# Performance work log

Measured on AMD Instinct MI355X. Metric: run time of the kernel, lower is better.

## Reference

```python
import jax, jax.numpy as jnp
import numpy as np

E, D, H, T = 8, 1024, 2816, 16384


def setup_inputs() -> dict:
    key = jax.random.key(0)
    k1, k2, k3, k4 = jax.random.split(key, 4)
    x = jax.random.normal(k1, (T, D), dtype=jnp.float32)
    # Params sized per init (w1/w3: [E, H, D], w2: [E, D, H]), trunc-normal-ish scale 0.02
    w1 = 0.02 * jax.random.normal(k2, (E, H, D), dtype=jnp.float32)
    w2 = 0.02 * jax.random.normal(k3, (E, D, H), dtype=jnp.float32)
    w3 = 0.02 * jax.random.normal(k4, (E, H, D), dtype=jnp.float32)
    # Per-expert token counts summing to < T (tail rows are padding, output zeros)
    rng = np.random.default_rng(0)
    props = rng.dirichlet(4.0 * np.ones(E))
    counts = np.floor(props * (T - 64)).astype(np.int32)
    num_tokens_per_expert = jnp.asarray(counts, dtype=jnp.int32)
    return {"x": x, "w1": w1, "w2": w2, "w3": w3,
            "num_tokens_per_expert": num_tokens_per_expert}


def reference(x, w1, w2, w3, num_tokens_per_expert):
    # Tokens are grouped contiguously by expert; grouped GEMM via lax.ragged_dot.
    g = num_tokens_per_expert.astype(jnp.int32)
    # rhs for ragged_dot must be [groups, k, n]
    h1 = jax.lax.ragged_dot(x, jnp.swapaxes(w1, 1, 2), g)   # [T, H] = x @ w1[e].T
    h3 = jax.lax.ragged_dot(x, jnp.swapaxes(w3, 1, 2), g)   # [T, H]
    h = jax.nn.silu(h1) * h3                                # SwiGLU
    out = jax.lax.ragged_dot(h, jnp.swapaxes(w2, 1, 2), g)  # [T, D]
    # Rows beyond sum(counts) are padding -> zeros, matching torch vstack of zeros
    valid = jnp.arange(x.shape[0]) < jnp.sum(g)
    return jnp.where(valid[:, None], out, jnp.zeros((), dtype=out.dtype))
```

## Files before the change

kernel.cpp:

```cpp
#include <hip/hip_runtime.h>

#define NE 8
#define DD 1024
#define HH 2816
#define TT 16384
#define MT (TT / 128 + NE)

constexpr int NJA = MT * (HH / 64);
constexpr int NJB = MT * (DD / 128);
constexpr int ZBLK = 64;

typedef __bf16 bf16;
typedef __bf16 bf16x4 __attribute__((ext_vector_type(4)));
typedef __bf16 bf16x8 __attribute__((ext_vector_type(8)));
typedef float f32x4 __attribute__((ext_vector_type(4)));

constexpr size_t HBUF_E = (size_t)TT * HH;
constexpr size_t XN = (size_t)TT * DD;
constexpr size_t WN = (size_t)NE * HH * DD;
constexpr size_t XB_OFF = HBUF_E * 2;
constexpr size_t W1B_OFF = XB_OFF + XN * 2;
constexpr size_t W3B_OFF = W1B_OFF + WN * 2;

__device__ __forceinline__ void gld16(const void* g, void* l) {
  __builtin_amdgcn_global_load_lds(
      (const __attribute__((address_space(1))) void*)g,
      (__attribute__((address_space(3))) void*)l, 16, 0, 0);
}

__device__ __forceinline__ f32x4 mfma16(bf16x8 a, bf16x8 b, f32x4 c) {
  return __builtin_amdgcn_mfma_f32_16x16x32_bf16(a, b, c, 0, 0, 0);
}

#define BARRIER()                      \
  do {                                 \
    __builtin_amdgcn_s_barrier();      \
    asm volatile("" ::: "memory");     \
  } while (0)

__global__ __launch_bounds__(256) void cvt3_k(
    const float4* __restrict__ x, const float4* __restrict__ w1,
    const float4* __restrict__ w3, bf16x4* __restrict__ xb,
    bf16x4* __restrict__ w1b, bf16x4* __restrict__ w3b) {
  constexpr int NBX = (int)(XN / 4 / 256);
  constexpr int NBW = (int)(WN / 4 / 256);
  int b = blockIdx.x;
  const float4* src;
  bf16x4* dst;
  int i;
  if (b < NBX) {
    src = x; dst = xb; i = b * 256 + threadIdx.x;
  } else if (b < NBX + NBW) {
    src = w1; dst = w1b; i = (b - NBX) * 256 + threadIdx.x;
  } else {
    src = w3; dst = w3b; i = (b - NBX - NBW) * 256 + threadIdx.x;
  }
  float4 v = src[i];
  bf16x4 o;
  o[0] = (bf16)v.x; o[1] = (bf16)v.y; o[2] = (bf16)v.z; o[3] = (bf16)v.w;
  dst[i] = o;
}

__global__ __launch_bounds__(256) void cvt_bf16_k(const float4* __restrict__ in,
                                                  bf16x4* __restrict__ out, int n4) {
  int i = blockIdx.x * 256 + threadIdx.x;
  if (i < n4) {
    float4 v = in[i];
    bf16x4 o;
    o[0] = (bf16)v.x; o[1] = (bf16)v.y; o[2] = (bf16)v.z; o[3] = (bf16)v.w;
    out[i] = o;
  }
}

struct TileInfo { int e, row0, rv; };
__device__ __forceinline__ TileInfo find_tile(const int* __restrict__ cnts, int t) {
  TileInfo ti; ti.e = -1; ti.row0 = 0; ti.rv = 0;
  int off = 0;
#pragma unroll
  for (int i = 0; i < NE; ++i) {
    int c = cnts[i];
    int tl = (c + 127) >> 7;
    if (ti.e < 0) {
      if (t < tl) {
        ti.e = i;
        ti.row0 = off + (t << 7);
        int rv = c - (t << 7);
        ti.rv = rv > 128 ? 128 : rv;
      } else {
        t -= tl;
      }
    }
    off += c;
  }
  return ti;
}

__global__ __launch_bounds__(256, 3) void swiglu_gemm_k(
    const bf16* __restrict__ x, const bf16* __restrict__ w1,
    const bf16* __restrict__ w3, const int* __restrict__ cnts,
    bf16* __restrict__ hbuf) {
  constexpr int NKT = DD / 32;

  int lin = blockIdx.x;
  lin = (lin & 7) * (NJA / 8) + (lin >> 3);
  const int tile = lin % MT;
  const int n0 = (lin / MT) * 64;
  TileInfo ti = find_tile(cnts, tile);
  if (ti.e < 0) return;

  const bf16* w1e = w1 + (size_t)ti.e * HH * DD;
  const bf16* w3e = w3 + (size_t)ti.e * HH * DD;
  const bf16* xb = x + (size_t)ti.row0 * DD;

  __shared__ bf16 sA[3][128 * 32];
  __shared__ bf16 sB1[3][64 * 32];
  __shared__ bf16 sB3[3][64 * 32];

  const int tid = threadIdx.x;
  const int lane = tid & 63, wave = tid >> 6;
  const int wm = wave >> 1, wn = wave & 1;
  const int lr = lane & 15, lkg = lane >> 4;

  const int r8 = tid >> 2;
  const int csw = (((tid & 3) ^ ((r8 >> 1) & 3)) << 3);
  const int rvm1 = ti.rv - 1;
  const int ra0 = r8 > rvm1 ? rvm1 : r8;
  const int ra1 = (64 + r8) > rvm1 ? rvm1 : 64 + r8;
  const bf16* gA0 = xb + (size_t)ra0 * DD + csw;
  const bf16* gA1 = xb + (size_t)ra1 * DD + csw;
  const bf16* gB1 = w1e + (size_t)(n0 + r8) * DD + csw;
  const bf16* gB3 = w3e + (size_t)(n0 + r8) * DD + csw;
  const int d0 = tid * 8, d1 = (256 + tid) * 8;

#define STAGE_A(kt, bb)                 \
  do {                                  \
    int kk = (kt) * 32;                 \
    gld16(gA0 + kk, &sA[bb][d0]);       \
    gld16(gA1 + kk, &sA[bb][d1]);       \
    gld16(gB1 + kk, &sB1[bb][d0]);      \
    gld16(gB3 + kk, &sB3[bb][d0]);      \
  } while (0)

  const int swz = (lkg ^ ((lr >> 1) & 3)) << 4;
  const int aoff = (wm * 64 + lr) * 64 + swz;
  const int boff = (wn * 32 + lr) * 64 + swz;

  f32x4 acc1[4][2], acc3[4][2];
#pragma unroll
  for (int i = 0; i < 4; ++i)
#pragma unroll
    for (int j = 0; j < 2; ++j) {
      acc1[i][j] = f32x4{0.f, 0.f, 0.f, 0.f};
      acc3[i][j] = f32x4{0.f, 0.f, 0.f, 0.f};
    }

  STAGE_A(0, 0);
  STAGE_A(1, 1);
  asm volatile("s_waitcnt vmcnt(4)" ::: "memory");
  BARRIER();

  int cur = 0;
  for (int kt = 0; kt < NKT; ++kt) {
    const bool pf = (kt + 2) < NKT;
    int nxt = cur + 2; if (nxt >= 3) nxt -= 3;
    if (pf) STAGE_A(kt + 2, nxt);

    const char* pA = (const char*)sA[cur];
    const char* pB1 = (const char*)sB1[cur];
    const char* pB3 = (const char*)sB3[cur];
    bf16x8 af[4], f1[2], f3[2];
#pragma unroll
    for (int mt = 0; mt < 4; ++mt)
      af[mt] = *(const bf16x8*)(pA + aoff + mt * 1024);
#pragma unroll
    for (int nt = 0; nt < 2; ++nt) {
      f1[nt] = *(const bf16x8*)(pB1 + boff + nt * 1024);
      f3[nt] = *(const bf16x8*)(pB3 + boff + nt * 1024);
    }
    __builtin_amdgcn_s_setprio(1);
#pragma unroll
    for (int mt = 0; mt < 4; ++mt)
#pragma unroll
      for (int nt = 0; nt < 2; ++nt) {
        acc1[mt][nt] = mfma16(f1[nt], af[mt], acc1[mt][nt]);
        acc3[mt][nt] = mfma16(f3[nt], af[mt], acc3[mt][nt]);
      }
    __builtin_amdgcn_s_setprio(0);
    if (pf) asm volatile("s_waitcnt vmcnt(4) lgkmcnt(0)" ::: "memory");
    else    asm volatile("s_waitcnt vmcnt(0) lgkmcnt(0)" ::: "memory");
    BARRIER();
    cur = (cur + 1 == 3) ? 0 : cur + 1;
  }
#undef STAGE_A

#pragma unroll
  for (int mt = 0; mt < 4; ++mt) {
    int row = wm * 64 + mt * 16 + lr;
    if (row < ti.rv) {
      size_t base = (size_t)(ti.row0 + row) * HH + n0 + wn * 32 + (lkg << 2);
#pragma unroll
      for (int nt = 0; nt < 2; ++nt) {
        bf16x4 o;
#pragma unroll
        for (int r = 0; r < 4; ++r) {
          float a = acc1[mt][nt][r], b = acc3[mt][nt][r];
          o[r] = (bf16)(a / (1.f + __expf(-a)) * b);
        }
        *(bf16x4*)&hbuf[base + nt * 16] = o;
      }
    }
  }
}

__global__ __launch_bounds__(256, 3) void down_gemm_k(
    const bf16* __restrict__ hbuf, const bf16* __restrict__ w2,
    const int* __restrict__ cnts, float* __restrict__ out) {
  constexpr int NKT = HH / 32;

  int b = blockIdx.x;
  if (b >= NJB) {
    int total = 0;
#pragma unroll
    for (int e = 0; e < NE; ++e) total += cnts[e];
    size_t base4 = (size_t)total * (DD / 4);
    size_t n4 = ((size_t)TT * DD) / 4 - base4;
    f32x4* o4 = (f32x4*)out + base4;
    f32x4 z{0.f, 0.f, 0.f, 0.f};
    for (size_t i = (size_t)(b - NJB) * 256 + threadIdx.x; i < n4;
         i += (size_t)ZBLK * 256)
      o4[i] = z;
    return;
  }

  int lin = (b & 7) * (NJB / 8) + (b >> 3);
  const int tile = lin % MT;
  const int n0 = (lin / MT) * 128;
  TileInfo ti = find_tile(cnts, tile);
  if (ti.e < 0) return;

  const bf16* w2e = w2 + (size_t)ti.e * DD * HH;
  const bf16* hb = hbuf + (size_t)ti.row0 * HH;

  __shared__ bf16 sA[3][128 * 32];
  __shared__ bf16 sB[3][128 * 32];

  const int tid = threadIdx.x;
  const int lane = tid & 63, wave = tid >> 6;
  const int wm = wave >> 1, wn = wave & 1;
  const int lr = lane & 15, lkg = lane >> 4;

  const int r8 = tid >> 2;
  const int csw = (((tid & 3) ^ ((r8 >> 1) & 3)) << 3);
  const int rvm1 = ti.rv - 1;
  const int ra0 = r8 > rvm1 ? rvm1 : r8;
  const int ra1 = (64 + r8) > rvm1 ? rvm1 : 64 + r8;
  const bf16* gA0 = hb + (size_t)ra0 * HH + csw;
  const bf16* gA1 = hb + (size_t)ra1 * HH + csw;
  const bf16* gB0 = w2e + (size_t)(n0 + r8) * HH + csw;
  const bf16* gB1 = w2e + (size_t)(n0 + 64 + r8) * HH + csw;
  const int d0 = tid * 8, d1 = (256 + tid) * 8;

#define STAGE_B(kt, bb)                 \
  do {                                  \
    int kk = (kt) * 32;                 \
    gld16(gA0 + kk, &sA[bb][d0]);       \
    gld16(gA1 + kk, &sA[bb][d1]);       \
    gld16(gB0 + kk, &sB[bb][d0]);       \
    gld16(gB1 + kk, &sB[bb][d1]);       \
  } while (0)

  const int swz = (lkg ^ ((lr >> 1) & 3)) << 4;
  const int aoff = (wm * 64 + lr) * 64 + swz;
  const int boff = (wn * 64 + lr) * 64 + swz;

  f32x4 acc[4][4];
#pragma unroll
  for (int i = 0; i < 4; ++i)
#pragma unroll
    for (int j = 0; j < 4; ++j) acc[i][j] = f32x4{0.f, 0.f, 0.f, 0.f};

  STAGE_B(0, 0);
  STAGE_B(1, 1);
  asm volatile("s_waitcnt vmcnt(4)" ::: "memory");
  BARRIER();

  int cur = 0;
  for (int kt = 0; kt < NKT; ++kt) {
    const bool pf = (kt + 2) < NKT;
    int nxt = cur + 2; if (nxt >= 3) nxt -= 3;
    if (pf) STAGE_B(kt + 2, nxt);

    const char* pA = (const char*)sA[cur];
    const char* pB = (const char*)sB[cur];
    bf16x8 af[4], bfm[4];
#pragma unroll
    for (int mt = 0; mt < 4; ++mt)
      af[mt] = *(const bf16x8*)(pA + aoff + mt * 1024);
#pragma unroll
    for (int nt = 0; nt < 4; ++nt)
      bfm[nt] = *(const bf16x8*)(pB + boff + nt * 1024);
    __builtin_amdgcn_s_setprio(1);
#pragma unroll
    for (int mt = 0; mt < 4; ++mt)
#pragma unroll
      for (int nt = 0; nt < 4; ++nt)
        acc[mt][nt] = mfma16(bfm[nt], af[mt], acc[mt][nt]);
    __builtin_amdgcn_s_setprio(0);
    if (pf) asm volatile("s_waitcnt vmcnt(4) lgkmcnt(0)" ::: "memory");
    else    asm volatile("s_waitcnt vmcnt(0) lgkmcnt(0)" ::: "memory");
    BARRIER();
    cur = (cur + 1 == 3) ? 0 : cur + 1;
  }
#undef STAGE_B

#pragma unroll
  for (int mt = 0; mt < 4; ++mt) {
    int row = wm * 64 + mt * 16 + lr;
    if (row < ti.rv) {
      size_t base = (size_t)(ti.row0 + row) * DD + n0 + wn * 64 + (lkg << 2);
#pragma unroll
      for (int nt = 0; nt < 4; ++nt)
        *(f32x4*)&out[base + nt * 16] = acc[mt][nt];
    }
  }
}

extern "C" void kernel_launch(void* const* d_in, const int* in_sizes, int n_in,
                              void* d_out, int out_size, void* d_ws, size_t ws_size,
                              hipStream_t stream) {
  const float* x = (const float*)d_in[0];
  const float* w1 = (const float*)d_in[1];
  const float* w2 = (const float*)d_in[2];
  const float* w3 = (const float*)d_in[3];
  const int* cnts = (const int*)d_in[4];
  float* out = (float*)d_out;

  char* ws = (char*)d_ws;
  bf16* hbuf = (bf16*)ws;
  bf16* xb = (bf16*)(ws + XB_OFF);
  bf16* w1b = (bf16*)(ws + W1B_OFF);
  bf16* w3b = (bf16*)(ws + W3B_OFF);
  bf16* w2b = w1b;

  constexpr int NBX = (int)(XN / 4 / 256);
  constexpr int NBW = (int)(WN / 4 / 256);

  cvt3_k<<<NBX + 2 * NBW, 256, 0, stream>>>((const float4*)x, (const float4*)w1,
                                            (const float4*)w3, (bf16x4*)xb,
                                            (bf16x4*)w1b, (bf16x4*)w3b);

  swiglu_gemm_k<<<NJA, 256, 0, stream>>>(xb, w1b, w3b, cnts, hbuf);

  cvt_bf16_k<<<NBW, 256, 0, stream>>>((const float4*)w2, (bf16x4*)w2b, (int)(WN / 4));

  down_gemm_k<<<NJB + ZBLK, 256, 0, stream>>>(hbuf, w2b, cnts, out);
}
```

Before: 740.5 us.

## Enlarge GEMM tiles to 8 waves with K=64 and split-phase prefetch

Both grouped GEMM kernels move from 256-thread blocks to 512-thread, 8-wave blocks. The output N tile doubles (128 for gate/up, 256 for down) and the K step grows from 32 to 64, with a new 8-way XOR swizzle. Each K iteration is split into two half-steps that interleave LDS fragment reads, half of the next prefetch, and MFMA bursts, separated by extra barriers. The aim is more operand reuse per byte loaded and fewer loop iterations. The costs are much more LDS per block, which lowers occupancy, more barriers per iteration, and coarser tiles that cause more waste on ragged expert tails.

```diff
diff --git a/kernel.cpp b/kernel.cpp
--- a/kernel.cpp
+++ b/kernel.cpp
@@ -6,8 +6,8 @@
 #define TT 16384
 #define MT (TT / 128 + NE)
 
-constexpr int NJA = MT * (HH / 64);
-constexpr int NJB = MT * (DD / 128);
+constexpr int NJA = MT * (HH / 128);
+constexpr int NJB = MT * (DD / 256);
 constexpr int ZBLK = 64;
 
 typedef __bf16 bf16;
@@ -95,16 +95,16 @@
   return ti;
 }
 
-__global__ __launch_bounds__(256, 3) void swiglu_gemm_k(
+__global__ __launch_bounds__(512, 2) void swiglu_gemm_k(
     const bf16* __restrict__ x, const bf16* __restrict__ w1,
     const bf16* __restrict__ w3, const int* __restrict__ cnts,
     bf16* __restrict__ hbuf) {
-  constexpr int NKT = DD / 32;
+  constexpr int NKT = DD / 64;
 
   int lin = blockIdx.x;
   lin = (lin & 7) * (NJA / 8) + (lin >> 3);
   const int tile = lin % MT;
-  const int n0 = (lin / MT) * 64;
+  const int n0 = (lin / MT) * 128;
   TileInfo ti = find_tile(cnts, tile);
   if (ti.e < 0) return;
 
@@ -112,38 +112,46 @@
   const bf16* w3e = w3 + (size_t)ti.e * HH * DD;
   const bf16* xb = x + (size_t)ti.row0 * DD;
 
-  __shared__ bf16 sA[3][128 * 32];
-  __shared__ bf16 sB1[3][64 * 32];
-  __shared__ bf16 sB3[3][64 * 32];
+  __shared__ bf16 sA[3][128 * 64];
+  __shared__ bf16 sB1[3][128 * 64];
+  __shared__ bf16 sB3[3][128 * 64];
 
   const int tid = threadIdx.x;
   const int lane = tid & 63, wave = tid >> 6;
-  const int wm = wave >> 1, wn = wave & 1;
-  const int lr = lane & 15, lkg = lane >> 4;
-
-  const int r8 = tid >> 2;
-  const int csw = (((tid & 3) ^ ((r8 >> 1) & 3)) << 3);
+  const int wm = wave >> 2, wn = wave & 3;
+  const int lr = lane & 15, lkg = (lane >> 4) & 3;
+
+  const int r8 = tid >> 3;
+  const int csw = ((tid & 7) ^ (r8 & 7)) << 3;
   const int rvm1 = ti.rv - 1;
   const int ra0 = r8 > rvm1 ? rvm1 : r8;
   const int ra1 = (64 + r8) > rvm1 ? rvm1 : 64 + r8;
   const bf16* gA0 = xb + (size_t)ra0 * DD + csw;
   const bf16* gA1 = xb + (size_t)ra1 * DD + csw;
-  const bf16* gB1 = w1e + (size_t)(n0 + r8) * DD + csw;
-  const bf16* gB3 = w3e + (size_t)(n0 + r8) * DD + csw;
-  const int d0 = tid * 8, d1 = (256 + tid) * 8;
-
-#define STAGE_A(kt, bb)                 \
-  do {                                  \
-    int kk = (kt) * 32;                 \
-    gld16(gA0 + kk, &sA[bb][d0]);       \
-    gld16(gA1 + kk, &sA[bb][d1]);       \
-    gld16(gB1 + kk, &sB1[bb][d0]);      \
-    gld16(gB3 + kk, &sB3[bb][d0]);      \
+  const bf16* gB1a = w1e + (size_t)(n0 + r8) * DD + csw;
+  const bf16* gB1b = w1e + (size_t)(n0 + 64 + r8) * DD + csw;
+  const bf16* gB3a = w3e + (size_t)(n0 + r8) * DD + csw;
+  const bf16* gB3b = w3e + (size_t)(n0 + 64 + r8) * DD + csw;
+  const int d0 = tid * 8, d1 = 4096 + tid * 8;
+
+#define STAGE_A_P0(kt, bb)               \
+  do {                                   \
+    int kk = (kt) * 64;                  \
+    gld16(gA0 + kk, &sA[bb][d0]);        \
+    gld16(gA1 + kk, &sA[bb][d1]);        \
+    gld16(gB1a + kk, &sB1[bb][d0]);      \
+    gld16(gB1b + kk, &sB1[bb][d1]);      \
   } while (0)
-
-  const int swz = (lkg ^ ((lr >> 1) & 3)) << 4;
-  const int aoff = (wm * 64 + lr) * 64 + swz;
-  const int boff = (wn * 32 + lr) * 64 + swz;
+#define STAGE_A_P1(kt, bb)               \
+  do {                                   \
+    int kk = (kt) * 64;                  \
+    gld16(gB3a + kk, &sB3[bb][d0]);      \
+    gld16(gB3b + kk, &sB3[bb][d1]);      \
+  } while (0)
+
+  const int s7 = lr & 7;
+  const int abase = (wm * 64 + lr) * 128 + ((lkg ^ s7) << 4);
+  const int bbase = (wn * 32 + lr) * 128 + ((lkg ^ s7) << 4);
 
   f32x4 acc1[4][2], acc3[4][2];
 #pragma unroll
@@ -154,29 +162,30 @@
       acc3[i][j] = f32x4{0.f, 0.f, 0.f, 0.f};
     }
 
-  STAGE_A(0, 0);
-  STAGE_A(1, 1);
-  asm volatile("s_waitcnt vmcnt(4)" ::: "memory");
+  STAGE_A_P0(0, 0); STAGE_A_P1(0, 0);
+  STAGE_A_P0(1, 1); STAGE_A_P1(1, 1);
+  asm volatile("s_waitcnt vmcnt(6)" ::: "memory");
   BARRIER();
 
   int cur = 0;
   for (int kt = 0; kt < NKT; ++kt) {
     const bool pf = (kt + 2) < NKT;
     int nxt = cur + 2; if (nxt >= 3) nxt -= 3;
-    if (pf) STAGE_A(kt + 2, nxt);
-
     const char* pA = (const char*)sA[cur];
     const char* pB1 = (const char*)sB1[cur];
     const char* pB3 = (const char*)sB3[cur];
+
     bf16x8 af[4], f1[2], f3[2];
 #pragma unroll
     for (int mt = 0; mt < 4; ++mt)
-      af[mt] = *(const bf16x8*)(pA + aoff + mt * 1024);
+      af[mt] = *(const bf16x8*)(pA + abase + mt * 2048);
 #pragma unroll
     for (int nt = 0; nt < 2; ++nt) {
-      f1[nt] = *(const bf16x8*)(pB1 + boff + nt * 1024);
-      f3[nt] = *(const bf16x8*)(pB3 + boff + nt * 1024);
-    }
+      f1[nt] = *(const bf16x8*)(pB1 + bbase + nt * 2048);
+      f3[nt] = *(const bf16x8*)(pB3 + bbase + nt * 2048);
+    }
+    if (pf) STAGE_A_P0(kt + 2, nxt);
+    BARRIER();
     __builtin_amdgcn_s_setprio(1);
 #pragma unroll
     for (int mt = 0; mt < 4; ++mt)
@@ -186,12 +195,34 @@
         acc3[mt][nt] = mfma16(f3[nt], af[mt], acc3[mt][nt]);
       }
     __builtin_amdgcn_s_setprio(0);
-    if (pf) asm volatile("s_waitcnt vmcnt(4) lgkmcnt(0)" ::: "memory");
-    else    asm volatile("s_waitcnt vmcnt(0) lgkmcnt(0)" ::: "memory");
+    BARRIER();
+
+#pragma unroll
+    for (int mt = 0; mt < 4; ++mt)
+      af[mt] = *(const bf16x8*)(pA + ((abase + mt * 2048) ^ 64));
+#pragma unroll
+    for (int nt = 0; nt < 2; ++nt) {
+      f1[nt] = *(const bf16x8*)(pB1 + ((bbase + nt * 2048) ^ 64));
+      f3[nt] = *(const bf16x8*)(pB3 + ((bbase + nt * 2048) ^ 64));
+    }
+    if (pf) STAGE_A_P1(kt + 2, nxt);
+    if (pf) asm volatile("s_waitcnt vmcnt(6)" ::: "memory");
+    else    asm volatile("s_waitcnt vmcnt(0)" ::: "memory");
+    BARRIER();
+    __builtin_amdgcn_s_setprio(1);
+#pragma unroll
+    for (int mt = 0; mt < 4; ++mt)
+#pragma unroll
+      for (int nt = 0; nt < 2; ++nt) {
+        acc1[mt][nt] = mfma16(f1[nt], af[mt], acc1[mt][nt]);
+        acc3[mt][nt] = mfma16(f3[nt], af[mt], acc3[mt][nt]);
+      }
+    __builtin_amdgcn_s_setprio(0);
     BARRIER();
     cur = (cur + 1 == 3) ? 0 : cur + 1;
   }
-#undef STAGE_A
+#undef STAGE_A_P0
+#undef STAGE_A_P1
 
 #pragma unroll
   for (int mt = 0; mt < 4; ++mt) {
@@ -212,10 +243,10 @@
   }
 }
 
-__global__ __launch_bounds__(256, 3) void down_gemm_k(
+__global__ __launch_bounds__(512, 2) void down_gemm_k(
     const bf16* __restrict__ hbuf, const bf16* __restrict__ w2,
     const int* __restrict__ cnts, float* __restrict__ out) {
-  constexpr int NKT = HH / 32;
+  constexpr int NKT = HH / 64;
 
   int b = blockIdx.x;
   if (b >= NJB) {
@@ -226,31 +257,31 @@
     size_t n4 = ((size_t)TT * DD) / 4 - base4;
     f32x4* o4 = (f32x4*)out + base4;
     f32x4 z{0.f, 0.f, 0.f, 0.f};
-    for (size_t i = (size_t)(b - NJB) * 256 + threadIdx.x; i < n4;
-         i += (size_t)ZBLK * 256)
+    for (size_t i = (size_t)(b - NJB) * 512 + threadIdx.x; i < n4;
+         i += (size_t)ZBLK * 512)
       o4[i] = z;
     return;
   }
 
   int lin = (b & 7) * (NJB / 8) + (b >> 3);
   const int tile = lin % MT;
-  const int n0 = (lin / MT) * 128;
+  const int n0 = (lin / MT) * 256;
   TileInfo ti = find_tile(cnts, tile);
   if (ti.e < 0) return;
 
   const bf16* w2e = w2 + (size_t)ti.e * DD * HH;
   const bf16* hb = hbuf + (size_t)ti.row0 * HH;
 
-  __shared__ bf16 sA[3][128 * 32];
-  __shared__ bf16 sB[3][128 * 32];
+  __shared__ bf16 sA[3][128 * 64];
+  __shared__ bf16 sB[3][256 * 64];
 
   const int tid = threadIdx.x;
   const int lane = tid & 63, wave = tid >> 6;
-  const int wm = wave >> 1, wn = wave & 1;
-  const int lr = lane & 15, lkg = lane >> 4;
-
-  const int r8 = tid >> 2;
-  const int csw = (((tid & 3) ^ ((r8 >> 1) & 3)) << 3);
+  const int wm = wave >> 2, wn = wave & 3;
+  const int lr = lane & 15, lkg = (lane >> 4) & 3;
+
+  const int r8 = tid >> 3;
+  const int csw = ((tid & 7) ^ (r8 & 7)) << 3;
   const int rvm1 = ti.rv - 1;
   const int ra0 = r8 > rvm1 ? rvm1 : r8;
   const int ra1 = (64 + r8) > rvm1 ? rvm1 : 64 + r8;
@@ -258,20 +289,29 @@
   const bf16* gA1 = hb + (size_t)ra1 * HH + csw;
   const bf16* gB0 = w2e + (size_t)(n0 + r8) * HH + csw;
   const bf16* gB1 = w2e + (size_t)(n0 + 64 + r8) * HH + csw;
-  const int d0 = tid * 8, d1 = (256 + tid) * 8;
-
-#define STAGE_B(kt, bb)                 \
-  do {                                  \
-    int kk = (kt) * 32;                 \
-    gld16(gA0 + kk, &sA[bb][d0]);       \
-    gld16(gA1 + kk, &sA[bb][d1]);       \
-    gld16(gB0 + kk, &sB[bb][d0]);       \
-    gld16(gB1 + kk, &sB[bb][d1]);       \
+  const bf16* gB2 = w2e + (size_t)(n0 + 128 + r8) * HH + csw;
+  const bf16* gB3 = w2e + (size_t)(n0 + 192 + r8) * HH + csw;
+  const int d0 = tid * 8, d1 = 4096 + tid * 8;
+  const int e2 = 8192 + tid * 8, e3 = 12288 + tid * 8;
+
+#define STAGE_B_P0(kt, bb)               \
+  do {                                   \
+    int kk = (kt) * 64;                  \
+    gld16(gA0 + kk, &sA[bb][d0]);        \
+    gld16(gA1 + kk, &sA[bb][d1]);        \
+    gld16(gB0 + kk, &sB[bb][d0]);        \
+    gld16(gB1 + kk, &sB[bb][d1]);        \
   } while (0)
-
-  const int swz = (lkg ^ ((lr >> 1) & 3)) << 4;
-  const int aoff = (wm * 64 + lr) * 64 + swz;
-  const int boff = (wn * 64 + lr) * 64 + swz;
+#define STAGE_B_P1(kt, bb)               \
+  do {                                   \
+    int kk = (kt) * 64;                  \
+    gld16(gB2 + kk, &sB[bb][e2]);        \
+    gld16(gB3 + kk, &sB[bb][e3]);        \
+  } while (0)
+
+  const int s7 = lr & 7;
+  const int abase = (wm * 64 + lr) * 128 + ((lkg ^ s7) << 4);
+  const int bbase = (wn * 64 + lr) * 128 + ((lkg ^ s7) << 4);
 
   f32x4 acc[4][4];
 #pragma unroll
@@ -279,26 +319,27 @@
 #pragma unroll
     for (int j = 0; j < 4; ++j) acc[i][j] = f32x4{0.f, 0.f, 0.f, 0.f};
 
-  STAGE_B(0, 0);
-  STAGE_B(1, 1);
-  asm volatile("s_waitcnt vmcnt(4)" ::: "memory");
+  STAGE_B_P0(0, 0); STAGE_B_P1(0, 0);
+  STAGE_B_P0(1, 1); STAGE_B_P1(1, 1);
+  asm volatile("s_waitcnt vmcnt(6)" ::: "memory");
   BARRIER();
 
   int cur = 0;
   for (int kt = 0; kt < NKT; ++kt) {
     const bool pf = (kt + 2) < NKT;
     int nxt = cur + 2; if (nxt >= 3) nxt -= 3;
-    if (pf) STAGE_B(kt + 2, nxt);
-
     const char* pA = (const char*)sA[cur];
     const char* pB = (const char*)sB[cur];
+
     bf16x8 af[4], bfm[4];
 #pragma unroll
     for (int mt = 0; mt < 4; ++mt)
-      af[mt] = *(const bf16x8*)(pA + aoff + mt * 1024);
+      af[mt] = *(const bf16x8*)(pA + abase + mt * 2048);
 #pragma unroll
     for (int nt = 0; nt < 4; ++nt)
-      bfm[nt] = *(const bf16x8*)(pB + boff + nt * 1024);
+      bfm[nt] = *(const bf16x8*)(pB + bbase + nt * 2048);
+    if (pf) STAGE_B_P0(kt + 2, nxt);
+    BARRIER();
     __builtin_amdgcn_s_setprio(1);
 #pragma unroll
     for (int mt = 0; mt < 4; ++mt)
@@ -306,12 +347,30 @@
       for (int nt = 0; nt < 4; ++nt)
         acc[mt][nt] = mfma16(bfm[nt], af[mt], acc[mt][nt]);
     __builtin_amdgcn_s_setprio(0);
-    if (pf) asm volatile("s_waitcnt vmcnt(4) lgkmcnt(0)" ::: "memory");
-    else    asm volatile("s_waitcnt vmcnt(0) lgkmcnt(0)" ::: "memory");
+    BARRIER();
+
+#pragma unroll
+    for (int mt = 0; mt < 4; ++mt)
+      af[mt] = *(const bf16x8*)(pA + ((abase + mt * 2048) ^ 64));
+#pragma unroll
+    for (int nt = 0; nt < 4; ++nt)
+      bfm[nt] = *(const bf16x8*)(pB + ((bbase + nt * 2048) ^ 64));
+    if (pf) STAGE_B_P1(kt + 2, nxt);
+    if (pf) asm volatile("s_waitcnt vmcnt(6)" ::: "memory");
+    else    asm volatile("s_waitcnt vmcnt(0)" ::: "memory");
+    BARRIER();
+    __builtin_amdgcn_s_setprio(1);
+#pragma unroll
+    for (int mt = 0; mt < 4; ++mt)
+#pragma unroll
+      for (int nt = 0; nt < 4; ++nt)
+        acc[mt][nt] = mfma16(bfm[nt], af[mt], acc[mt][nt]);
+    __builtin_amdgcn_s_setprio(0);
     BARRIER();
     cur = (cur + 1 == 3) ? 0 : cur + 1;
   }
-#undef STAGE_B
+#undef STAGE_B_P0
+#undef STAGE_B_P1
 
 #pragma unroll
   for (int mt = 0; mt < 4; ++mt) {
@@ -349,9 +408,9 @@
                                             (const float4*)w3, (bf16x4*)xb,
                                             (bf16x4*)w1b, (bf16x4*)w3b);
 
-  swiglu_gemm_k<<<NJA, 256, 0, stream>>>(xb, w1b, w3b, cnts, hbuf);
+  swiglu_gemm_k<<<NJA, 512, 0, stream>>>(xb, w1b, w3b, cnts, hbuf);
 
   cvt_bf16_k<<<NBW, 256, 0, stream>>>((const float4*)w2, (bf16x4*)w2b, (int)(WN / 4));
 
-  down_gemm_k<<<NJB + ZBLK, 256, 0, stream>>>(hbuf, w2b, cnts, out);
-}
+  down_gemm_k<<<NJB + ZBLK, 512, 0, stream>>>(hbuf, w2b, cnts, out);
+}
```

After: 758.3 us. 1.02x slower.
